# Performance work log

Measured on AMD Instinct MI355X. Metric: run time of the kernel, lower is better.

Reference implementation:

```python
import jax, jax.numpy as jnp
import numpy as np

UNITS = 128

def setup_inputs() -> dict:
    key = jax.random.key(0)
    ks = jax.random.split(key, 8)
    B, T, U = 2048, 200, UNITS
    s = 1.0 / np.sqrt(U)
    inp = {
        'inputs': jax.random.normal(ks[0], (B, T, U + 1), dtype=jnp.float32),
        'h0': jnp.zeros((B, U), dtype=jnp.float32),
        'W_r': jax.random.normal(ks[1], (U, U), dtype=jnp.float32) * s,
        'U_r': jax.random.normal(ks[2], (U, U), dtype=jnp.float32) * s,
        'b_r': jnp.zeros((U,), dtype=jnp.float32),
        'W_z': jax.random.normal(ks[3], (U, U), dtype=jnp.float32) * s,
        'U_z': jax.random.normal(ks[4], (U, U), dtype=jnp.float32) * s,
        'b_z': jnp.zeros((U,), dtype=jnp.float32),
        'W_h': jax.random.normal(ks[5], (U, U), dtype=jnp.float32) * s,
        'U_h': jax.random.normal(ks[6], (U, U), dtype=jnp.float32) * s,
        'b_h': jnp.zeros((U,), dtype=jnp.float32),
    }
    # attention weights a in [0,1]
    a = jax.nn.sigmoid(inp['inputs'][..., U:])
    inp['inputs'] = jnp.concatenate([inp['inputs'][..., :U], a], axis=-1)
    return inp


def reference(inputs, h0, W_r, U_r, b_r, W_z, U_z, b_z, W_h, U_h, b_h):
    U = W_r.shape[0]
    x = inputs[..., :U]          # [B, T, U]
    a = inputs[..., U:]          # [B, T, 1] attention scores
    # Precompute input-side gate projections for all timesteps (one big GEMM each)
    xr = jnp.einsum('btu,uv->btv', x, W_r) + b_r
    xz = jnp.einsum('btu,uv->btv', x, W_z) + b_z
    xh = jnp.einsum('btu,uv->btv', x, W_h) + b_h
    # time-major for scan
    xs = (jnp.swapaxes(xr, 0, 1), jnp.swapaxes(xz, 0, 1),
          jnp.swapaxes(xh, 0, 1), jnp.swapaxes(a, 0, 1))

    def step(h_prev, ts):
        xr_t, xz_t, xh_t, a_t = ts
        r = jax.nn.sigmoid(xr_t + h_prev @ U_r)
        u = jax.nn.sigmoid(xz_t + h_prev @ U_z)
        h_tilda = jnp.tanh(xh_t + r * (h_prev @ U_h))
        u_hat = a_t * u
        h = (1.0 - u_hat) * h_prev + u_hat * h_tilda
        return h, h

    _, hs = jax.lax.scan(step, h0, xs)      # hs: [T, B, U]
    return jnp.swapaxes(hs, 0, 1)           # [B, T, U]
```

## Files before the change

kernel.cpp:

```cpp
#include <hip/hip_runtime.h>
#include <hip/hip_bf16.h>

#define TSTEPS 200
#define RS 25800

typedef __attribute__((ext_vector_type(8))) short short8;
typedef __attribute__((ext_vector_type(4))) float f32x4;
typedef __attribute__((ext_vector_type(4), aligned(4))) float f32x4u;

__device__ __forceinline__ short f2bf(float f){
  return (short)__builtin_bit_cast(unsigned short, __float2bfloat16(f));
}
__device__ __forceinline__ float bf2f(short s){
  unsigned u = ((unsigned)(unsigned short)s) << 16;
  return __builtin_bit_cast(float, u);
}
__device__ __forceinline__ float sigm(float x){ return 1.0f/(1.0f + __expf(-x)); }
__device__ __forceinline__ float tanh_(float x){ return 1.0f - 2.0f/(1.0f + __expf(2.0f*x)); }

#define MFMA16(a,b,c) __builtin_amdgcn_mfma_f32_16x16x32_bf16((a),(b),(c),0,0,0)

#define HSTR 136

__global__ __launch_bounds__(256, 1) void gru_fused(
    const float* __restrict__ inp, const float* __restrict__ h0,
    const float* __restrict__ Wr, const float* __restrict__ Ur, const float* __restrict__ br,
    const float* __restrict__ Wz, const float* __restrict__ Uz, const float* __restrict__ bz,
    const float* __restrict__ Wh, const float* __restrict__ Uh, const float* __restrict__ bh,
    float* __restrict__ out)
{
  __shared__ short hlds[2][2][16*HSTR];

  const int tid  = threadIdx.x;
  const int lane = tid & 63;
  const int w    = tid >> 6;
  const int l15  = lane & 15;
  const int l4   = lane >> 4;
  const int b0   = blockIdx.x * 16;

  short8 BW[6][2][4];
  {
    const float* Wm[6] = {Wr, Ur, Wz, Uz, Wh, Uh};
    #pragma unroll
    for (int m = 0; m < 6; ++m)
      #pragma unroll
      for (int tl = 0; tl < 2; ++tl)
        #pragma unroll
        for (int kk = 0; kk < 4; ++kk){
          short8 f;
          #pragma unroll
          for (int e = 0; e < 8; ++e)
            f[e] = f2bf(Wm[m][(size_t)(kk*32 + l4*8 + e)*128 + (w*32 + tl*16 + l15)]);
          BW[m][tl][kk] = f;
        }
  }

  float bR[2], bZ[2], bH[2];
  #pragma unroll
  for (int tl = 0; tl < 2; ++tl){
    int c = w*32 + tl*16 + l15;
    bR[tl] = br[c]; bZ[tl] = bz[c]; bH[tl] = bh[c];
  }

  float hprev[2][4];
  #pragma unroll
  for (int tl = 0; tl < 2; ++tl)
    #pragma unroll
    for (int j = 0; j < 4; ++j){
      int row = l4*4 + j;
      int col = w*32 + tl*16 + l15;
      float h = h0[(size_t)(b0+row)*128 + col];
      hprev[tl][j] = h;
      short hi = f2bf(h);
      short lo = f2bf(h - bf2f(hi));
      hlds[0][0][row*HSTR + col] = hi;
      hlds[0][1][row*HSTR + col] = lo;
    }

  const float* xbase = inp + (size_t)(b0 + l15)*RS + l4*8;
  f32x4 xb[4][2];
  float abuf[4];
  #pragma unroll
  for (int kk = 0; kk < 4; ++kk){
    xb[kk][0] = *(const f32x4u*)(xbase + kk*32);
    xb[kk][1] = *(const f32x4u*)(xbase + kk*32 + 4);
  }
  #pragma unroll
  for (int j = 0; j < 4; ++j)
    abuf[j] = inp[(size_t)(b0 + l4*4 + j)*RS + 128];

  __syncthreads();

  for (int t = 0; t < TSTEPS; ++t){
    short8 xf[4];
    #pragma unroll
    for (int kk = 0; kk < 4; ++kk){
      short8 f;
      #pragma unroll
      for (int e = 0; e < 4; ++e) f[e]   = f2bf(xb[kk][0][e]);
      #pragma unroll
      for (int e = 0; e < 4; ++e) f[4+e] = f2bf(xb[kk][1][e]);
      xf[kk] = f;
    }
    float acur[4];
    #pragma unroll
    for (int j = 0; j < 4; ++j) acur[j] = abuf[j];

    {
      int tn = (t < TSTEPS-1) ? (t+1) : t;
      const float* p = xbase + (size_t)tn*129;
      #pragma unroll
      for (int kk = 0; kk < 4; ++kk){
        xb[kk][0] = *(const f32x4u*)(p + kk*32);
        xb[kk][1] = *(const f32x4u*)(p + kk*32 + 4);
      }
      #pragma unroll
      for (int j = 0; j < 4; ++j)
        abuf[j] = inp[(size_t)(b0 + l4*4 + j)*RS + (size_t)tn*129 + 128];
    }

    const short* hbhi = &hlds[t&1][0][0];
    const short* hblo = &hlds[t&1][1][0];
    short8 hhi[4], hlo4[4];
    {
      int base = l15*HSTR + l4*8;
      #pragma unroll
      for (int kk = 0; kk < 4; ++kk){
        hhi[kk]  = *(const short8*)(hbhi + base + kk*32);
        hlo4[kk] = *(const short8*)(hblo + base + kk*32);
      }
    }

    f32x4 aR[2], aZ[2], aXH[2], aHH[2];
    #pragma unroll
    for (int tl = 0; tl < 2; ++tl){
      f32x4 r0, z0, x0, h0v;
      r0[0]=r0[1]=r0[2]=r0[3]=bR[tl];
      z0[0]=z0[1]=z0[2]=z0[3]=bZ[tl];
      x0[0]=x0[1]=x0[2]=x0[3]=bH[tl];
      h0v[0]=h0v[1]=h0v[2]=h0v[3]=0.0f;
      aR[tl]=r0; aZ[tl]=z0; aXH[tl]=x0; aHH[tl]=h0v;
    }
    #pragma unroll
    for (int tl = 0; tl < 2; ++tl){
      #pragma unroll
      for (int kk = 0; kk < 4; ++kk){
        aR[tl]  = MFMA16(xf[kk],   BW[0][tl][kk], aR[tl]);
        aZ[tl]  = MFMA16(xf[kk],   BW[2][tl][kk], aZ[tl]);
        aXH[tl] = MFMA16(xf[kk],   BW[4][tl][kk], aXH[tl]);
        aR[tl]  = MFMA16(hhi[kk],  BW[1][tl][kk], aR[tl]);
        aZ[tl]  = MFMA16(hhi[kk],  BW[3][tl][kk], aZ[tl]);
        aHH[tl] = MFMA16(hhi[kk],  BW[5][tl][kk], aHH[tl]);
        aR[tl]  = MFMA16(hlo4[kk], BW[1][tl][kk], aR[tl]);
        aZ[tl]  = MFMA16(hlo4[kk], BW[3][tl][kk], aZ[tl]);
        aHH[tl] = MFMA16(hlo4[kk], BW[5][tl][kk], aHH[tl]);
      }
    }

    short* nxhi = &hlds[(t+1)&1][0][0];
    short* nxlo = &hlds[(t+1)&1][1][0];
    #pragma unroll
    for (int tl = 0; tl < 2; ++tl)
      #pragma unroll
      for (int j = 0; j < 4; ++j){
        int row = l4*4 + j;
        int col = w*32 + tl*16 + l15;
        float r  = sigm(aR[tl][j]);
        float z  = sigm(aZ[tl][j]);
        float ht = tanh_(aXH[tl][j] + r*aHH[tl][j]);
        float uh = acur[j]*z;
        float hp = hprev[tl][j];
        float h  = hp + uh*(ht - hp);
        hprev[tl][j] = h;
        out[((size_t)(b0+row)*TSTEPS + t)*128 + col] = h;
        short hi = f2bf(h);
        short lo = f2bf(h - bf2f(hi));
        nxhi[row*HSTR + col] = hi;
        nxlo[row*HSTR + col] = lo;
      }
    __syncthreads();
  }
}

extern "C" void kernel_launch(void* const* d_in, const int* in_sizes, int n_in,
                              void* d_out, int out_size, void* d_ws, size_t ws_size,
                              hipStream_t stream)
{
  (void)in_sizes; (void)n_in; (void)d_ws; (void)ws_size; (void)out_size;
  gru_fused<<<128, 256, 0, stream>>>(
      (const float*)d_in[0], (const float*)d_in[1],
      (const float*)d_in[2], (const float*)d_in[3], (const float*)d_in[4],
      (const float*)d_in[5], (const float*)d_in[6], (const float*)d_in[7],
      (const float*)d_in[8], (const float*)d_in[9], (const float*)d_in[10],
      (float*)d_out);
}
```

Baseline: 728.4 us.

## Split GRU columns across eight waves and use fast reciprocal in gates

```diff
diff --git a/kernel.cpp b/kernel.cpp
--- a/kernel.cpp
+++ b/kernel.cpp
@@ -15,14 +15,15 @@
   unsigned u = ((unsigned)(unsigned short)s) << 16;
   return __builtin_bit_cast(float, u);
 }
-__device__ __forceinline__ float sigm(float x){ return 1.0f/(1.0f + __expf(-x)); }
-__device__ __forceinline__ float tanh_(float x){ return 1.0f - 2.0f/(1.0f + __expf(2.0f*x)); }
+__device__ __forceinline__ float rcpf_(float x){ return __builtin_amdgcn_rcpf(x); }
+__device__ __forceinline__ float sigm(float x){ return rcpf_(1.0f + __expf(-x)); }
+__device__ __forceinline__ float tanh_(float x){ return 1.0f - 2.0f*rcpf_(1.0f + __expf(2.0f*x)); }
 
 #define MFMA16(a,b,c) __builtin_amdgcn_mfma_f32_16x16x32_bf16((a),(b),(c),0,0,0)
 
 #define HSTR 136
 
-__global__ __launch_bounds__(256, 1) void gru_fused(
+__global__ __launch_bounds__(512, 2) void gru_fused(
     const float* __restrict__ inp, const float* __restrict__ h0,
     const float* __restrict__ Wr, const float* __restrict__ Ur, const float* __restrict__ br,
     const float* __restrict__ Wz, const float* __restrict__ Uz, const float* __restrict__ bz,
@@ -37,45 +38,36 @@
   const int l15  = lane & 15;
   const int l4   = lane >> 4;
   const int b0   = blockIdx.x * 16;
+  const int col  = w*16 + l15;
 
-  short8 BW[6][2][4];
+  short8 BW[6][4];
   {
     const float* Wm[6] = {Wr, Ur, Wz, Uz, Wh, Uh};
     #pragma unroll
     for (int m = 0; m < 6; ++m)
       #pragma unroll
-      for (int tl = 0; tl < 2; ++tl)
+      for (int kk = 0; kk < 4; ++kk){
+        short8 f;
         #pragma unroll
-        for (int kk = 0; kk < 4; ++kk){
-          short8 f;
-          #pragma unroll
-          for (int e = 0; e < 8; ++e)
-            f[e] = f2bf(Wm[m][(size_t)(kk*32 + l4*8 + e)*128 + (w*32 + tl*16 + l15)]);
-          BW[m][tl][kk] = f;
-        }
+        for (int e = 0; e < 8; ++e)
+          f[e] = f2bf(Wm[m][(size_t)(kk*32 + l4*8 + e)*128 + col]);
+        BW[m][kk] = f;
+      }
   }
 
-  float bR[2], bZ[2], bH[2];
+  const float bR = br[col], bZ = bz[col], bH = bh[col];
+
+  float hprev[4];
   #pragma unroll
-  for (int tl = 0; tl < 2; ++tl){
-    int c = w*32 + tl*16 + l15;
-    bR[tl] = br[c]; bZ[tl] = bz[c]; bH[tl] = bh[c];
+  for (int j = 0; j < 4; ++j){
+    int row = l4*4 + j;
+    float h = h0[(size_t)(b0+row)*128 + col];
+    hprev[j] = h;
+    short hi = f2bf(h);
+    short lo = f2bf(h - bf2f(hi));
+    hlds[0][0][row*HSTR + col] = hi;
+    hlds[0][1][row*HSTR + col] = lo;
   }
-
-  float hprev[2][4];
-  #pragma unroll
-  for (int tl = 0; tl < 2; ++tl)
-    #pragma unroll
-    for (int j = 0; j < 4; ++j){
-      int row = l4*4 + j;
-      int col = w*32 + tl*16 + l15;
-      float h = h0[(size_t)(b0+row)*128 + col];
-      hprev[tl][j] = h;
-      short hi = f2bf(h);
-      short lo = f2bf(h - bf2f(hi));
-      hlds[0][0][row*HSTR + col] = hi;
-      hlds[0][1][row*HSTR + col] = lo;
-    }
 
   const float* xbase = inp + (size_t)(b0 + l15)*RS + l4*8;
   f32x4 xb[4][2];
@@ -92,6 +84,18 @@
   __syncthreads();
 
   for (int t = 0; t < TSTEPS; ++t){
+    const short* hbhi = &hlds[t&1][0][0];
+    const short* hblo = &hlds[t&1][1][0];
+    short8 hhi[4], hlo4[4];
+    {
+      int base = l15*HSTR + l4*8;
+      #pragma unroll
+      for (int kk = 0; kk < 4; ++kk){
+        hhi[kk]  = *(const short8*)(hbhi + base + kk*32);
+        hlo4[kk] = *(const short8*)(hblo + base + kk*32);
+      }
+    }
+
     short8 xf[4];
     #pragma unroll
     for (int kk = 0; kk < 4; ++kk){
@@ -119,65 +123,46 @@
         abuf[j] = inp[(size_t)(b0 + l4*4 + j)*RS + (size_t)tn*129 + 128];
     }
 
-    const short* hbhi = &hlds[t&1][0][0];
-    const short* hblo = &hlds[t&1][1][0];
-    short8 hhi[4], hlo4[4];
-    {
-      int base = l15*HSTR + l4*8;
-      #pragma unroll
-      for (int kk = 0; kk < 4; ++kk){
-        hhi[kk]  = *(const short8*)(hbhi + base + kk*32);
-        hlo4[kk] = *(const short8*)(hblo + base + kk*32);
-      }
-    }
+    f32x4 aR, aZ, aXH, aHH;
+    aR[0]=aR[1]=aR[2]=aR[3]=bR;
+    aZ[0]=aZ[1]=aZ[2]=aZ[3]=bZ;
+    aXH[0]=aXH[1]=aXH[2]=aXH[3]=bH;
+    aHH[0]=aHH[1]=aHH[2]=aHH[3]=0.0f;
 
-    f32x4 aR[2], aZ[2], aXH[2], aHH[2];
     #pragma unroll
-    for (int tl = 0; tl < 2; ++tl){
-      f32x4 r0, z0, x0, h0v;
-      r0[0]=r0[1]=r0[2]=r0[3]=bR[tl];
-      z0[0]=z0[1]=z0[2]=z0[3]=bZ[tl];
-      x0[0]=x0[1]=x0[2]=x0[3]=bH[tl];
-      h0v[0]=h0v[1]=h0v[2]=h0v[3]=0.0f;
-      aR[tl]=r0; aZ[tl]=z0; aXH[tl]=x0; aHH[tl]=h0v;
+    for (int kk = 0; kk < 4; ++kk){
+      aR  = MFMA16(xf[kk], BW[0][kk], aR);
+      aZ  = MFMA16(xf[kk], BW[2][kk], aZ);
+      aXH = MFMA16(xf[kk], BW[4][kk], aXH);
     }
     #pragma unroll
-    for (int tl = 0; tl < 2; ++tl){
-      #pragma unroll
-      for (int kk = 0; kk < 4; ++kk){
-        aR[tl]  = MFMA16(xf[kk],   BW[0][tl][kk], aR[tl]);
-        aZ[tl]  = MFMA16(xf[kk],   BW[2][tl][kk], aZ[tl]);
-        aXH[tl] = MFMA16(xf[kk],   BW[4][tl][kk], aXH[tl]);
-        aR[tl]  = MFMA16(hhi[kk],  BW[1][tl][kk], aR[tl]);
-        aZ[tl]  = MFMA16(hhi[kk],  BW[3][tl][kk], aZ[tl]);
-        aHH[tl] = MFMA16(hhi[kk],  BW[5][tl][kk], aHH[tl]);
-        aR[tl]  = MFMA16(hlo4[kk], BW[1][tl][kk], aR[tl]);
-        aZ[tl]  = MFMA16(hlo4[kk], BW[3][tl][kk], aZ[tl]);
-        aHH[tl] = MFMA16(hlo4[kk], BW[5][tl][kk], aHH[tl]);
-      }
+    for (int kk = 0; kk < 4; ++kk){
+      aR  = MFMA16(hhi[kk],  BW[1][kk], aR);
+      aZ  = MFMA16(hhi[kk],  BW[3][kk], aZ);
+      aHH = MFMA16(hhi[kk],  BW[5][kk], aHH);
+      aR  = MFMA16(hlo4[kk], BW[1][kk], aR);
+      aZ  = MFMA16(hlo4[kk], BW[3][kk], aZ);
+      aHH = MFMA16(hlo4[kk], BW[5][kk], aHH);
     }
 
     short* nxhi = &hlds[(t+1)&1][0][0];
     short* nxlo = &hlds[(t+1)&1][1][0];
     #pragma unroll
-    for (int tl = 0; tl < 2; ++tl)
-      #pragma unroll
-      for (int j = 0; j < 4; ++j){
-        int row = l4*4 + j;
-        int col = w*32 + tl*16 + l15;
-        float r  = sigm(aR[tl][j]);
-        float z  = sigm(aZ[tl][j]);
-        float ht = tanh_(aXH[tl][j] + r*aHH[tl][j]);
-        float uh = acur[j]*z;
-        float hp = hprev[tl][j];
-        float h  = hp + uh*(ht - hp);
-        hprev[tl][j] = h;
-        out[((size_t)(b0+row)*TSTEPS + t)*128 + col] = h;
-        short hi = f2bf(h);
-        short lo = f2bf(h - bf2f(hi));
-        nxhi[row*HSTR + col] = hi;
-        nxlo[row*HSTR + col] = lo;
-      }
+    for (int j = 0; j < 4; ++j){
+      int row = l4*4 + j;
+      float r  = sigm(aR[j]);
+      float z  = sigm(aZ[j]);
+      float ht = tanh_(aXH[j] + r*aHH[j]);
+      float uh = acur[j]*z;
+      float hp = hprev[j];
+      float h  = hp + uh*(ht - hp);
+      hprev[j] = h;
+      out[((size_t)(b0+row)*TSTEPS + t)*128 + col] = h;
+      short hi = f2bf(h);
+      short lo = f2bf(h - bf2f(hi));
+      nxhi[row*HSTR + col] = hi;
+      nxlo[row*HSTR + col] = lo;
+    }
     __syncthreads();
   }
 }
@@ -187,7 +172,7 @@
                               hipStream_t stream)
 {
   (void)in_sizes; (void)n_in; (void)d_ws; (void)ws_size; (void)out_size;
-  gru_fused<<<128, 256, 0, stream>>>(
+  gru_fused<<<128, 512, 0, stream>>>(
       (const float*)d_in[0], (const float*)d_in[1],
       (const float*)d_in[2], (const float*)d_in[3], (const float*)d_in[4],
       (const float*)d_in[5], (const float*)d_in[6], (const float*)d_in[7],
```

Measured after the change: 648.6 us. -11.0%, faster.
